# Kernel optimization log

Hardware: AMD Instinct MI355X
Metric: run time of the kernel (lower is better)

Reference implementation:

```python
import jax, jax.numpy as jnp
import numpy as np

N_HEADS = 8
HEAD_DIM = 64
SCALE = HEAD_DIM ** -0.5


def setup_inputs() -> dict:
    key = jax.random.key(0)
    k1, k2, k3 = jax.random.split(key, 3)
    B, C, Hs, Ws = 8, 512, 64, 64
    x = jax.random.normal(k1, (B, C, Hs, Ws), dtype=jnp.float32)
    _h = jnp.zeros((1,), dtype=jnp.int32)  # unused arg in original forward
    # proj_in: Linear(C, 3*H*hd); stored as (in, out) so y = x @ W + b
    W_in = jax.random.normal(k2, (C, 3 * N_HEADS * HEAD_DIM), dtype=jnp.float32) * (C ** -0.5)
    b_in = jnp.zeros((3 * N_HEADS * HEAD_DIM,), dtype=jnp.float32)
    W_out = jax.random.normal(k3, (N_HEADS * HEAD_DIM, C), dtype=jnp.float32) * ((N_HEADS * HEAD_DIM) ** -0.5)
    b_out = jnp.zeros((C,), dtype=jnp.float32)
    return {"x": x, "_h": _h, "W_in": W_in, "b_in": b_in, "W_out": W_out, "b_out": b_out}


def reference(x, _h, W_in, b_in, W_out, b_out):
    in_shape = x.shape
    B, C = in_shape[0], in_shape[1]
    # (B, C, *spatial) -> (B, S, C)
    xf = x.reshape(B, C, -1).transpose(0, 2, 1)
    S = xf.shape[1]
    # fused QKV projection -> (B, S, H, 3*hd), chunk into q, k, v: (B, S, H, hd)
    qkv = (xf @ W_in + b_in).reshape(B, S, N_HEADS, 3 * HEAD_DIM)
    q, k, v = jnp.split(qkv, 3, axis=-1)
    # NOTE: faithful to the original, SDPA receives (B, S, H, hd) WITHOUT a
    # transpose to (B, H, S, hd): attention runs over the heads axis (HxH),
    # batched over (B, S).
    scores = jnp.einsum("bsqd,bskd->bsqk", q, k) * SCALE  # (B, S, H, H)
    attn = jax.nn.softmax(scores, axis=-1)
    out = jnp.einsum("bsqk,bskd->bsqd", attn, v)  # (B, S, H, hd)
    out = out.reshape(B, S, N_HEADS * HEAD_DIM)
    out = out @ W_out + b_out  # (B, S, C)
    return out.transpose(0, 2, 1).reshape(in_shape)
```

## Files before the change

### kernel.cpp

```cpp
#include <hip/hip_runtime.h>
#include <hip/hip_bf16.h>

typedef __attribute__((ext_vector_type(8))) short bh8;
typedef __attribute__((ext_vector_type(4))) float fx4;

#define GLOAD16(g, l)                                                          \
  __builtin_amdgcn_global_load_lds(                                            \
      (const __attribute__((address_space(1))) void*)(g),                      \
      (__attribute__((address_space(3))) void*)(l), 16, 0, 0)

__device__ __forceinline__ unsigned short f2bf(float f) {
  unsigned int u = __float_as_uint(f);
  u += 0x7fffu + ((u >> 16) & 1u);
  return (unsigned short)(u >> 16);
}
__device__ __forceinline__ float bf2f(short h) {
  return __uint_as_float(((unsigned int)(unsigned short)h) << 16);
}

__global__ __launch_bounds__(256) void transpose_cvt(
    const float* __restrict__ in, short* __restrict__ out, int R, int Ccols) {
  __shared__ float tile[64][65];
  const int b = blockIdx.z;
  const int c0 = blockIdx.x * 64;
  const int r0 = blockIdx.y * 64;
  const float* ip = in + (size_t)b * R * Ccols;
  short* op = out + (size_t)b * Ccols * R;
  const int tid = threadIdx.x;
  const int tx = tid & 63, ty = tid >> 6;
#pragma unroll
  for (int i = 0; i < 16; ++i) {
    int r = ty + i * 4;
    tile[tx][r] = ip[(size_t)(r0 + r) * Ccols + c0 + tx];
  }
  __syncthreads();
  const int cg = tid & 15;
  const int rr = tid >> 4;
#pragma unroll
  for (int i = 0; i < 4; ++i) {
    const int cc = i * 16 + rr;
    const unsigned int lo = (unsigned int)f2bf(tile[cc][cg * 4 + 0]) |
                            ((unsigned int)f2bf(tile[cc][cg * 4 + 1]) << 16);
    const unsigned int hi = (unsigned int)f2bf(tile[cc][cg * 4 + 2]) |
                            ((unsigned int)f2bf(tile[cc][cg * 4 + 3]) << 16);
    uint2 v; v.x = lo; v.y = hi;
    *(uint2*)&op[(size_t)(c0 + cc) * R + r0 + cg * 4] = v;
  }
}

template <int MODE>
__global__ __launch_bounds__(256) void gemm_bt(
    const short* __restrict__ A, const short* __restrict__ Bt,
    const float* __restrict__ bias, void* __restrict__ Cout,
    int M, int N, int K, int tok0) {
  __shared__ short As[2][128 * 32] __attribute__((aligned(16)));
  __shared__ short Bs[2][128 * 32] __attribute__((aligned(16)));
  const int tid = threadIdx.x;
  const int lane = tid & 63;
  const int wv = tid >> 6;
  const int wr = wv >> 1, wc = wv & 1;

  const int nbx = gridDim.x, nby = gridDim.y;
  const int nwg = nbx * nby;
  int h = blockIdx.y * nbx + blockIdx.x;
  int L = h;
  if ((nwg & 7) == 0) {
    const int q = nwg >> 3;
    L = (h & 7) * q + (h >> 3);
  }
  int bx, by;
  if (MODE == 1) {
    by = L / nbx;
    bx = L - by * nbx;
  } else {
    bx = L / nby;
    by = L - bx * nby;
  }
  const int m0 = by * 128, n0 = bx * 128;

  const int lr = lane & 15;
  const int lk = (lane >> 4) * 8;
  const int rsw = ((lr >> 1) & 3) << 3;

  fx4 acc[4][4] = {};

  const int srow = tid >> 2;
  const int skoff = (((tid & 3) ^ ((tid >> 3) & 3)) * 8);
  const size_t abase = (size_t)(m0 + srow) * K + skoff;
  const size_t bbase = (size_t)(n0 + srow) * K + skoff;
  const int ldoff = wv * 1024;

  {
    char* lA = (char*)As[0] + ldoff;
    char* lB = (char*)Bs[0] + ldoff;
    GLOAD16(A + abase, lA);
    GLOAD16(A + abase + (size_t)64 * K, lA + 4096);
    GLOAD16(Bt + bbase, lB);
    GLOAD16(Bt + bbase + (size_t)64 * K, lB + 4096);
  }
  __syncthreads();

  int cur = 0;
  for (int k0 = 0; k0 < K; k0 += 32) {
    if (k0 + 32 < K) {
      char* lA = (char*)As[cur ^ 1] + ldoff;
      char* lB = (char*)Bs[cur ^ 1] + ldoff;
      GLOAD16(A + abase + k0 + 32, lA);
      GLOAD16(A + abase + (size_t)64 * K + k0 + 32, lA + 4096);
      GLOAD16(Bt + bbase + k0 + 32, lB);
      GLOAD16(Bt + bbase + (size_t)64 * K + k0 + 32, lB + 4096);
    }

    bh8 af[4], bfm[4];
#pragma unroll
    for (int i = 0; i < 4; ++i) {
      af[i] = *(const bh8*)&As[cur][(wr * 64 + i * 16 + lr) * 32 + (lk ^ rsw)];
      bfm[i] = *(const bh8*)&Bs[cur][(wc * 64 + i * 16 + lr) * 32 + (lk ^ rsw)];
    }
#pragma unroll
    for (int i = 0; i < 4; ++i)
#pragma unroll
      for (int j = 0; j < 4; ++j)
        acc[i][j] = __builtin_amdgcn_mfma_f32_16x16x32_bf16(af[i], bfm[j],
                                                            acc[i][j], 0, 0, 0);

    __syncthreads();
    cur ^= 1;
  }

  if (MODE == 1) {
    short* C = (short*)Cout;
#pragma unroll
    for (int i = 0; i < 4; ++i) {
      const int gm = m0 + wr * 64 + i * 16 + (lane >> 4) * 4;
#pragma unroll
      for (int j = 0; j < 4; ++j) {
        const int gn = n0 + wc * 64 + j * 16 + lr;
        const float bv = bias[gn];
#pragma unroll
        for (int r = 0; r < 4; ++r)
          C[(size_t)(gm + r) * N + gn] = (short)f2bf(acc[i][j][r] + bv);
      }
    }
  } else {
    float* C = (float*)Cout;
#pragma unroll
    for (int i = 0; i < 4; ++i) {
      const int ch0 = m0 + wr * 64 + i * 16 + (lane >> 4) * 4;
#pragma unroll
      for (int j = 0; j < 4; ++j) {
        const int t = tok0 + n0 + wc * 64 + j * 16 + lr;
        const int bb = t >> 12, s = t & 4095;
#pragma unroll
        for (int r = 0; r < 4; ++r) {
          const int ch = ch0 + r;
          C[((size_t)(bb * 512 + ch)) * 4096 + s] = acc[i][j][r] + bias[ch];
        }
      }
    }
  }
}

__global__ __launch_bounds__(256) void attn_kernel(
    const short* __restrict__ QKV, short* __restrict__ AO) {
  __shared__ short sq[4][1536] __attribute__((aligned(16)));
  const int tid = threadIdx.x, lane = tid & 63, wv = tid >> 6;
  const int t = blockIdx.x * 4 + wv;

  {
    const short* g = QKV + (size_t)t * 1536 + lane * 8;
    char* l = (char*)&sq[wv][0];
    GLOAD16(g, l);
    GLOAD16(g + 512, l + 1024);
    GLOAD16(g + 1024, l + 2048);
  }
  asm volatile("s_waitcnt vmcnt(0)" ::: "memory");

  const int i = lane >> 3, j = lane & 7;
  const short* q = &sq[wv][i * 192];
  const short* k = &sq[wv][j * 192 + 64];
  float s = 0.f;
#pragma unroll
  for (int c = 0; c < 8; ++c) {
    bh8 qa = *(const bh8*)&q[c * 8];
    bh8 ka = *(const bh8*)&k[c * 8];
#pragma unroll
    for (int e = 0; e < 8; ++e) s += bf2f(qa[e]) * bf2f(ka[e]);
  }
  s *= 0.125f;

  float m = s;
  m = fmaxf(m, __shfl_xor(m, 1));
  m = fmaxf(m, __shfl_xor(m, 2));
  m = fmaxf(m, __shfl_xor(m, 4));
  float p = __expf(s - m);
  float sum = p;
  sum += __shfl_xor(sum, 1);
  sum += __shfl_xor(sum, 2);
  sum += __shfl_xor(sum, 4);
  const float a = p / sum;

  float o[8] = {};
#pragma unroll
  for (int jj = 0; jj < 8; ++jj) {
    const float aj = __shfl(a, (lane & 56) | jj);
    bh8 va = *(const bh8*)&sq[wv][jj * 192 + 128 + j * 8];
#pragma unroll
    for (int e = 0; e < 8; ++e) o[e] += aj * bf2f(va[e]);
  }
  bh8 ov;
#pragma unroll
  for (int e = 0; e < 8; ++e) ov[e] = (short)f2bf(o[e]);
  *(bh8*)&AO[(size_t)t * 512 + i * 64 + j * 8] = ov;
}

extern "C" void kernel_launch(void* const* d_in, const int* in_sizes, int n_in,
                              void* d_out, int out_size, void* d_ws,
                              size_t ws_size, hipStream_t stream) {
  const float* x = (const float*)d_in[0];
  const float* W_in = (const float*)d_in[2];
  const float* b_in = (const float*)d_in[3];
  const float* W_out = (const float*)d_in[4];
  const float* b_out = (const float*)d_in[5];
  float* out = (float*)d_out;

  short* Xbf = (short*)d_ws;
  short* WinT = Xbf + (size_t)32768 * 512;
  short* WoutT = WinT + (size_t)1536 * 512;
  short* QKVc = WoutT + (size_t)512 * 512;

  const size_t fixed_bytes =
      ((size_t)32768 * 512 + (size_t)1536 * 512 + (size_t)512 * 512) * 2;
  int NC = 1;
  while (NC < 256 &&
         fixed_bytes + ((size_t)32768 / NC) * 1536 * 2 > ws_size)
    NC <<= 1;
  const int Mc = 32768 / NC;

  transpose_cvt<<<dim3(64, 8, 8), 256, 0, stream>>>(x, Xbf, 512, 4096);
  transpose_cvt<<<dim3(24, 8, 1), 256, 0, stream>>>(W_in, WinT, 512, 1536);
  transpose_cvt<<<dim3(8, 8, 1), 256, 0, stream>>>(W_out, WoutT, 512, 512);

  for (int c = 0; c < NC; ++c) {
    const int t0 = c * Mc;
    short* Ach = Xbf + (size_t)t0 * 512;
    gemm_bt<1><<<dim3(12, Mc / 128), 256, 0, stream>>>(Ach, WinT, b_in, QKVc,
                                                       Mc, 1536, 512, 0);
    attn_kernel<<<dim3(Mc / 4), 256, 0, stream>>>(QKVc, Ach);
    gemm_bt<2><<<dim3(Mc / 128, 4), 256, 0, stream>>>(WoutT, Ach, b_out, out,
                                                      512, Mc, 512, t0);
  }
}
```

Measured before the change: 253.9 us.

## Use triple-buffered LDS pipeline with one barrier per k-step in GEMM

Replaces the double-buffered GEMM main loop with a three-slot LDS ring that prefetches two k-tiles ahead. Uses explicit vmcnt waits and a single s_barrier per iteration instead of two __syncthreads. K is made a compile-time template parameter so the loop can be unrolled and addressing simplified. This is meant to hide global-load latency better and cut synchronisation, at the cost of more LDS per block (48KB), which may lower occupancy.

Measured after the change: 243.7 us. -4.0%, faster.

```diff
diff --git a/kernel.cpp b/kernel.cpp
--- a/kernel.cpp
+++ b/kernel.cpp
@@ -48,13 +48,14 @@
   }
 }
 
-template <int MODE>
+template <int MODE, int KC>
 __global__ __launch_bounds__(256) void gemm_bt(
     const short* __restrict__ A, const short* __restrict__ Bt,
     const float* __restrict__ bias, void* __restrict__ Cout,
-    int M, int N, int K, int tok0) {
-  __shared__ short As[2][128 * 32] __attribute__((aligned(16)));
-  __shared__ short Bs[2][128 * 32] __attribute__((aligned(16)));
+    int M, int N, int tok0) {
+  __shared__ short As[3][128 * 32] __attribute__((aligned(16)));
+  __shared__ short Bs[3][128 * 32] __attribute__((aligned(16)));
+  constexpr int NT = KC / 32;
   const int tid = threadIdx.x;
   const int lane = tid & 63;
   const int wv = tid >> 6;
@@ -86,36 +87,41 @@
 
   const int srow = tid >> 2;
   const int skoff = (((tid & 3) ^ ((tid >> 3) & 3)) * 8);
-  const size_t abase = (size_t)(m0 + srow) * K + skoff;
-  const size_t bbase = (size_t)(n0 + srow) * K + skoff;
+  const size_t abase = (size_t)(m0 + srow) * KC + skoff;
+  const size_t bbase = (size_t)(n0 + srow) * KC + skoff;
   const int ldoff = wv * 1024;
 
-  {
-    char* lA = (char*)As[0] + ldoff;
-    char* lB = (char*)Bs[0] + ldoff;
-    GLOAD16(A + abase, lA);
-    GLOAD16(A + abase + (size_t)64 * K, lA + 4096);
-    GLOAD16(Bt + bbase, lB);
-    GLOAD16(Bt + bbase + (size_t)64 * K, lB + 4096);
-  }
-  __syncthreads();
-
-  int cur = 0;
-  for (int k0 = 0; k0 < K; k0 += 32) {
-    if (k0 + 32 < K) {
-      char* lA = (char*)As[cur ^ 1] + ldoff;
-      char* lB = (char*)Bs[cur ^ 1] + ldoff;
-      GLOAD16(A + abase + k0 + 32, lA);
-      GLOAD16(A + abase + (size_t)64 * K + k0 + 32, lA + 4096);
-      GLOAD16(Bt + bbase + k0 + 32, lB);
-      GLOAD16(Bt + bbase + (size_t)64 * K + k0 + 32, lB + 4096);
-    }
-
+  auto STAGE = [&](int kt, int slot) {
+    const size_t ko = (size_t)kt * 32;
+    char* lA = (char*)As[slot] + ldoff;
+    char* lB = (char*)Bs[slot] + ldoff;
+    GLOAD16(A + abase + ko, lA);
+    GLOAD16(A + abase + (size_t)64 * KC + ko, lA + 4096);
+    GLOAD16(Bt + bbase + ko, lB);
+    GLOAD16(Bt + bbase + (size_t)64 * KC + ko, lB + 4096);
+  };
+
+  STAGE(0, 0);
+  STAGE(1, 1);
+
+  for (int t = 0; t < NT; ++t) {
+    __builtin_amdgcn_sched_barrier(0);
+    if (t < NT - 1) {
+      asm volatile("s_waitcnt vmcnt(4)" ::: "memory");
+    } else {
+      asm volatile("s_waitcnt vmcnt(0)" ::: "memory");
+    }
+    __builtin_amdgcn_s_barrier();
+    __builtin_amdgcn_sched_barrier(0);
+    if (t + 2 < NT) STAGE(t + 2, (t + 2) % 3);
+    __builtin_amdgcn_sched_barrier(0);
+
+    const int sl = t % 3;
     bh8 af[4], bfm[4];
 #pragma unroll
     for (int i = 0; i < 4; ++i) {
-      af[i] = *(const bh8*)&As[cur][(wr * 64 + i * 16 + lr) * 32 + (lk ^ rsw)];
-      bfm[i] = *(const bh8*)&Bs[cur][(wc * 64 + i * 16 + lr) * 32 + (lk ^ rsw)];
+      af[i] = *(const bh8*)&As[sl][(wr * 64 + i * 16 + lr) * 32 + (lk ^ rsw)];
+      bfm[i] = *(const bh8*)&Bs[sl][(wc * 64 + i * 16 + lr) * 32 + (lk ^ rsw)];
     }
 #pragma unroll
     for (int i = 0; i < 4; ++i)
@@ -123,9 +129,6 @@
       for (int j = 0; j < 4; ++j)
         acc[i][j] = __builtin_amdgcn_mfma_f32_16x16x32_bf16(af[i], bfm[j],
                                                             acc[i][j], 0, 0, 0);
-
-    __syncthreads();
-    cur ^= 1;
   }
 
   if (MODE == 1) {
@@ -244,10 +247,10 @@
   for (int c = 0; c < NC; ++c) {
     const int t0 = c * Mc;
     short* Ach = Xbf + (size_t)t0 * 512;
-    gemm_bt<1><<<dim3(12, Mc / 128), 256, 0, stream>>>(Ach, WinT, b_in, QKVc,
-                                                       Mc, 1536, 512, 0);
+    gemm_bt<1, 512><<<dim3(12, Mc / 128), 256, 0, stream>>>(Ach, WinT, b_in,
+                                                            QKVc, Mc, 1536, 0);
     attn_kernel<<<dim3(Mc / 4), 256, 0, stream>>>(QKVc, Ach);
-    gemm_bt<2><<<dim3(Mc / 128, 4), 256, 0, stream>>>(WoutT, Ach, b_out, out,
-                                                      512, Mc, 512, t0);
-  }
-}
+    gemm_bt<2, 512><<<dim3(Mc / 128, 4), 256, 0, stream>>>(WoutT, Ach, b_out,
+                                                           out, 512, Mc, t0);
+  }
+}
```
